# Optimization experiments

Hardware: AMD Instinct MI355X
Metric: run time of the kernel (lower is better)

The kernel has to match this reference:

```python
import jax, jax.numpy as jnp
import numpy as np

B, S, D = 2, 2048, 1024
H, HD = 16, 64  # num_attention_heads, attention_head_size


def setup_inputs() -> dict:
    key = jax.random.key(0)
    ks = jax.random.split(key, 8)
    std = 0.02
    return {
        "hidden_states": jax.random.normal(ks[0], (B, S, D), dtype=jnp.float32),
        "attention_mask": jnp.zeros((B, 1, 1, S), dtype=jnp.float32),
        "Wq": jax.random.normal(ks[1], (D, D), dtype=jnp.float32) * std,
        "bq": jnp.zeros((D,), dtype=jnp.float32),
        "Wk": jax.random.normal(ks[2], (D, D), dtype=jnp.float32) * std,
        "bk": jnp.zeros((D,), dtype=jnp.float32),
        "Wv": jax.random.normal(ks[3], (D, D), dtype=jnp.float32) * std,
        "bv": jnp.zeros((D,), dtype=jnp.float32),
    }


def reference(hidden_states, attention_mask, Wq, bq, Wk, bk, Wv, bv):
    b, s, d = hidden_states.shape

    def split_heads(x):  # [b,s,D] -> [b,H,s,HD]
        return x.reshape(b, s, H, HD).transpose(0, 2, 1, 3)

    q = split_heads(hidden_states @ Wq + bq)
    k = split_heads(hidden_states @ Wk + bk)
    v = split_heads(hidden_states @ Wv + bv)

    scores = jnp.einsum("bhqd,bhkd->bhqk", q, k) / jnp.sqrt(jnp.float32(HD))
    scores = scores + attention_mask  # additive mask, broadcast [b,1,1,s]
    probs = jax.nn.softmax(scores, axis=-1)  # dropout is identity at inference
    ctx = jnp.einsum("bhqk,bhkd->bhqd", probs, v)
    out = ctx.transpose(0, 2, 1, 3).reshape(b, s, d)
    return out
```

## Files before the change

### kernel.cpp

```cpp
#include <hip/hip_runtime.h>
#include <math.h>

#define CB 2
#define CS 2048
#define CD 1024
#define CH 16
#define CHD 64
#define CM (CB*CS)

#define QSCALE 0.18033688f
#define LOG2E  1.44269504f
#define BLOG   40.0f

typedef unsigned short u16;
using bf16x8 = __attribute__((ext_vector_type(8))) short;
using u16x8  = __attribute__((ext_vector_type(8))) unsigned short;
using f32x4  = __attribute__((ext_vector_type(4))) float;

__device__ __forceinline__ u16 f2bf(float f) {
    unsigned int u = __float_as_uint(f);
    u = (u + 0x7FFFu + ((u >> 16) & 1u)) >> 16;
    return (u16)u;
}

__device__ __forceinline__ unsigned cvt_pk_bf16(float lo, float hi) {
    unsigned r;
    asm("v_cvt_pk_bf16_f32 %0, %1, %2" : "=v"(r) : "v"(lo), "v"(hi));
    return r;
}

__device__ __forceinline__ void load_lds16(const u16* g, u16* l) {
    __builtin_amdgcn_global_load_lds(
        (const __attribute__((address_space(1))) unsigned int*)g,
        (__attribute__((address_space(3))) unsigned int*)l, 16, 0, 0);
}

__global__ __launch_bounds__(256)
void convert_all(const float* __restrict__ X, u16* __restrict__ Xb,
                 const float* __restrict__ Wq, const float* __restrict__ Wk,
                 const float* __restrict__ Wv, u16* __restrict__ Wt)
{
    const int bid = blockIdx.x;
    const int tid = threadIdx.x;

    if (bid < 2048) {
        size_t i = ((size_t)bid * 256 + tid) * 8;
        float4 v0 = *(const float4*)(X + i);
        float4 v1 = *(const float4*)(X + i + 4);
        u16x8 o;
        o[0] = f2bf(v0.x); o[1] = f2bf(v0.y); o[2] = f2bf(v0.z); o[3] = f2bf(v0.w);
        o[4] = f2bf(v1.x); o[5] = f2bf(v1.y); o[6] = f2bf(v1.z); o[7] = f2bf(v1.w);
        *(u16x8*)(Xb + i) = o;
        return;
    }

    const int r3 = bid - 2048;
    const int z  = r3 >> 8;
    const int bx = r3 & 15;
    const int by = (r3 >> 4) & 15;
    const float* W = (z == 0) ? Wq : (z == 1) ? Wk : Wv;
    const float sc = (z == 0) ? QSCALE : 1.0f;
    u16* Wo = Wt + (size_t)z * CD * CD;

    __shared__ u16 T[64][72];
    const int k0 = bx << 6;
    const int n0 = by << 6;

    #pragma unroll
    for (int it = 0; it < 4; ++it) {
        int r = (tid >> 4) + (it << 4);
        int c = (tid & 15) << 2;
        float4 v = *(const float4*)(W + (size_t)(k0 + r) * CD + n0 + c);
        T[c + 0][r] = f2bf(v.x * sc);
        T[c + 1][r] = f2bf(v.y * sc);
        T[c + 2][r] = f2bf(v.z * sc);
        T[c + 3][r] = f2bf(v.w * sc);
    }
    __syncthreads();
    #pragma unroll
    for (int it = 0; it < 2; ++it) {
        int cc = tid + (it << 8);
        int n  = cc >> 3;
        int ch = (cc & 7) << 3;
        *(uint4*)(Wo + (size_t)(n0 + n) * CD + k0 + ch) = *(const uint4*)&T[n][ch];
    }
}

__global__ __launch_bounds__(256, 4)
void qkv_gemm_mfma(const u16* __restrict__ Xb, const u16* __restrict__ Wt,
                   const float* __restrict__ bq, const float* __restrict__ bk,
                   const float* __restrict__ bv,
                   u16* __restrict__ Qb, u16* __restrict__ Kb,
                   u16* __restrict__ Vt)
{
    const int flat = blockIdx.x + (blockIdx.y << 5) + (blockIdx.z << 8);
    const int nf   = (flat & 7) * 96 + (flat >> 3);
    const int bx   = nf & 31;
    const int by   = (nf >> 5) & 7;
    const int z    = nf >> 8;

    const u16* W = Wt + (size_t)z * CD * CD;
    const float* bias = (z == 0) ? bq : (z == 1) ? bk : bv;
    const float bscale = (z == 0) ? QSCALE : 1.0f;

    __shared__ u16 smem[17408];
    u16* As = smem;
    u16* Bs = smem + 8192;

    const int tid  = threadIdx.x;
    const int w    = tid >> 6;
    const int l    = tid & 63;
    const int l15  = l & 15;
    const int quad = l >> 4;
    const int wm   = w >> 1;
    const int wn   = w & 1;

    const int row0 = bx << 7;
    const int n0   = by << 7;

    f32x4 acc[4][4];
    #pragma unroll
    for (int mi = 0; mi < 4; ++mi)
        #pragma unroll
        for (int nt = 0; nt < 4; ++nt)
            acc[mi][nt] = (f32x4){0.f, 0.f, 0.f, 0.f};

    const u16* Ag = Xb + (size_t)row0 * CD;
    const u16* Bg = W  + (size_t)n0   * CD;
    const int lr8 = l >> 3;
    const int ls  = l & 7;
    const int lg  = (ls ^ lr8) << 3;
    const int q7  = l15 & 7;

    for (int k0 = 0; k0 < CD; k0 += 64) {
        __syncthreads();
        #pragma unroll
        for (int i = 0; i < 4; ++i) {
            int r = w * 32 + 8 * i + lr8;
            load_lds16(Ag + (size_t)r * CD + k0 + lg, As + (size_t)(w * 32 + 8 * i) * 64);
            load_lds16(Bg + (size_t)r * CD + k0 + lg, Bs + (size_t)(w * 32 + 8 * i) * 64);
        }
        __syncthreads();

        #pragma unroll
        for (int kk = 0; kk < 2; ++kk) {
            bf16x8 af[4], bfr[4];
            #pragma unroll
            for (int mi = 0; mi < 4; ++mi)
                af[mi] = *(const bf16x8*)
                    &As[(wm * 64 + mi * 16 + l15) * 64 + (((kk * 4 + quad) ^ q7) << 3)];
            #pragma unroll
            for (int nt = 0; nt < 4; ++nt)
                bfr[nt] = *(const bf16x8*)
                    &Bs[(wn * 64 + nt * 16 + l15) * 64 + (((kk * 4 + quad) ^ q7) << 3)];
            #pragma unroll
            for (int mi = 0; mi < 4; ++mi)
                #pragma unroll
                for (int nt = 0; nt < 4; ++nt)
                    acc[mi][nt] = __builtin_amdgcn_mfma_f32_16x16x32_bf16(
                        af[mi], bfr[nt], acc[mi][nt], 0, 0, 0);
        }
    }

    __syncthreads();

    u16 (*Ct)[136] = (u16(*)[136])smem;

    if (z < 2) {
        u16* Og = (z == 0) ? Qb : Kb;
        float bb[4];
        #pragma unroll
        for (int nt = 0; nt < 4; ++nt)
            bb[nt] = bias[n0 + wn * 64 + nt * 16 + l15] * bscale;

        #pragma unroll
        for (int nt = 0; nt < 4; ++nt)
            #pragma unroll
            for (int mi = 0; mi < 4; ++mi)
                #pragma unroll
                for (int r = 0; r < 4; ++r)
                    Ct[wm * 64 + mi * 16 + quad * 4 + r][wn * 64 + nt * 16 + l15] =
                        f2bf(acc[mi][nt][r] + bb[nt]);
        __syncthreads();
        #pragma unroll
        for (int it = 0; it < 8; ++it) {
            int c  = tid + (it << 8);
            int rl = c >> 4;
            int ck = c & 15;
            uint4 d = *(const uint4*)&Ct[rl][ck * 8];
            int gcol = n0 + ck * 8;
            int h = gcol >> 6, hd = gcol & 63;
            int m = row0 + rl;
            int b = m >> 11, s = m & (CS - 1);
            *(uint4*)(Og + ((size_t)(b * CH + h) * CS + s) * CHD + hd) = d;
        }
    } else {
        #pragma unroll
        for (int nt = 0; nt < 4; ++nt) {
            int col = n0 + wn * 64 + nt * 16 + l15;
            float bb = bias[col];
            #pragma unroll
            for (int mi = 0; mi < 4; ++mi)
                #pragma unroll
                for (int r = 0; r < 4; ++r) {
                    int ml = wm * 64 + mi * 16 + quad * 4 + r;
                    Ct[wn * 64 + nt * 16 + l15][ml] = f2bf(acc[mi][nt][r] + bb);
                }
        }
        __syncthreads();
        #pragma unroll
        for (int it = 0; it < 8; ++it) {
            int c   = tid + (it << 8);
            int dvl = c >> 4;
            int ch  = c & 15;
            uint4 vdat = *(const uint4*)&Ct[dvl][ch * 8];
            int col = n0 + dvl;
            int h   = col >> 6;
            int dv  = col & 63;
            int m0  = row0 + ch * 8;
            int b   = m0 >> 11;
            int s0  = m0 & (CS - 1);
            *(uint4*)(Vt + (((size_t)(b * CH + h)) * CHD + dv) * CS + s0) = vdat;
        }
    }
}

__global__ __launch_bounds__(512, 4)
void attn_mfma(const u16* __restrict__ Qg, const u16* __restrict__ Kg,
               const u16* __restrict__ Vtg, const float* __restrict__ mask,
               float* __restrict__ out)
{
    __shared__ u16 smem[32768];
    u16* KstB = smem;
    u16* VstB = smem + 8192;
    u16* PlB  = smem + 16384;

    const int flat = blockIdx.y * 16 + blockIdx.x;
    const int nf   = ((flat & 7) << 6) + (flat >> 3);
    const int q0   = (nf & 15) << 7;
    const int bh   = nf >> 4;
    const int b    = bh >> 4;
    const int h    = bh & 15;

    const int tid = threadIdx.x;
    const int w    = tid >> 6;
    const int qh   = w & 3;
    const int kh   = w >> 2;
    const int l    = tid & 63;
    const int l15  = l & 15;
    const int quad = l >> 4;
    const int q7   = l15 & 7;
    const int lr8  = l >> 3;
    const int lg   = ((l & 7) ^ lr8) << 3;

    const u16* Qp     = Qg  + (size_t)bh * CS * CHD;
    const u16* Kph    = Kg  + (size_t)bh * CS * CHD + ((size_t)(kh << 10)) * CHD;
    const u16* Vph    = Vtg + (size_t)bh * CHD * CS + (kh << 10);
    const float* mrh  = mask + (size_t)b * CS + (kh << 10);

    u16* Kst = KstB + kh * 4096;
    u16* Vst = VstB + kh * 4096;
    u16* Pw  = PlB  + w * 2048;

    bf16x8 qf[2][2];
    #pragma unroll
    for (int nq = 0; nq < 2; ++nq)
        #pragma unroll
        for (int hh = 0; hh < 2; ++hh)
            qf[nq][hh] = *(const bf16x8*)(
                Qp + (size_t)(q0 + qh * 32 + nq * 16 + l15) * CHD + hh * 32 + quad * 8);

    float lsum[2] = {0.f, 0.f};
    f32x4 O[2][4];
    #pragma unroll
    for (int nq = 0; nq < 2; ++nq)
        #pragma unroll
        for (int dt = 0; dt < 4; ++dt)
            O[nq][dt] = (f32x4){0.f, 0.f, 0.f, 0.f};

    for (int kt = 0; kt < 16; ++kt) {
        const int k0 = kt << 6;
        __syncthreads();
        #pragma unroll
        for (int i = 0; i < 2; ++i) {
            int rl = qh * 16 + 8 * i;
            load_lds16(Kph + (size_t)(k0 + rl + lr8) * CHD + lg, &Kst[rl * 64]);
            load_lds16(Vph + (size_t)(rl + lr8) * CS + k0 + lg,  &Vst[rl * 64]);
        }
        __syncthreads();

        bf16x8 kf[4][2];
        #pragma unroll
        for (int mt = 0; mt < 4; ++mt)
            #pragma unroll
            for (int hh = 0; hh < 2; ++hh)
                kf[mt][hh] = *(const bf16x8*)
                    &Kst[(mt * 16 + l15) * 64 + (((hh * 4 + quad) ^ q7) << 3)];

        f32x4 mc[4];
        #pragma unroll
        for (int mt = 0; mt < 4; ++mt) {
            f32x4 mv = *(const f32x4*)(mrh + k0 + mt * 16 + quad * 4);
            #pragma unroll
            for (int r = 0; r < 4; ++r)
                mc[mt][r] = fmaf(mv[r], LOG2E, -BLOG);
        }

        #pragma unroll
        for (int nq = 0; nq < 2; ++nq) {
            f32x4 st[4];
            #pragma unroll
            for (int mt = 0; mt < 4; ++mt) {
                f32x4 c0 = mc[mt];
                c0 = __builtin_amdgcn_mfma_f32_16x16x32_bf16(kf[mt][0], qf[nq][0], c0, 0, 0, 0);
                st[mt] = __builtin_amdgcn_mfma_f32_16x16x32_bf16(kf[mt][1], qf[nq][1], c0, 0, 0, 0);
            }
            float rs = lsum[nq];
            #pragma unroll
            for (int mt = 0; mt < 4; ++mt) {
                #pragma unroll
                for (int r = 0; r < 4; ++r) {
                    st[mt][r] = exp2f(st[mt][r]);
                    rs += st[mt][r];
                }
                int g = 2 * mt + (quad >> 1);
                int addr = (nq * 16 + l15) * 64 + ((g ^ q7) << 3) + ((quad & 1) << 2);
                uint2 d;
                d.x = cvt_pk_bf16(st[mt][0], st[mt][1]);
                d.y = cvt_pk_bf16(st[mt][2], st[mt][3]);
                *(uint2*)&Pw[addr] = d;
            }
            lsum[nq] = rs;
        }

        bf16x8 pf[2][2];
        #pragma unroll
        for (int nq = 0; nq < 2; ++nq)
            #pragma unroll
            for (int hh = 0; hh < 2; ++hh)
                pf[nq][hh] = *(const bf16x8*)
                    &Pw[(nq * 16 + l15) * 64 + (((hh * 4 + quad) ^ q7) << 3)];

        bf16x8 vf[4][2];
        #pragma unroll
        for (int dt = 0; dt < 4; ++dt)
            #pragma unroll
            for (int hh = 0; hh < 2; ++hh)
                vf[dt][hh] = *(const bf16x8*)
                    &Vst[(dt * 16 + l15) * 64 + (((hh * 4 + quad) ^ q7) << 3)];

        #pragma unroll
        for (int nq = 0; nq < 2; ++nq)
            #pragma unroll
            for (int dt = 0; dt < 4; ++dt) {
                O[nq][dt] = __builtin_amdgcn_mfma_f32_16x16x32_bf16(
                    pf[nq][0], vf[dt][0], O[nq][dt], 0, 0, 0);
                O[nq][dt] = __builtin_amdgcn_mfma_f32_16x16x32_bf16(
                    pf[nq][1], vf[dt][1], O[nq][dt], 0, 0, 0);
            }
    }

    #pragma unroll
    for (int nq = 0; nq < 2; ++nq) {
        lsum[nq] += __shfl_xor(lsum[nq], 16);
        lsum[nq] += __shfl_xor(lsum[nq], 32);
    }

    __syncthreads();
    float* ob   = (float*)smem;
    float* lbuf = (float*)PlB;

    if (kh == 1) {
        float* obw = ob + qh * 2048;
        #pragma unroll
        for (int nq = 0; nq < 2; ++nq)
            #pragma unroll
            for (int dt = 0; dt < 4; ++dt)
                #pragma unroll
                for (int r = 0; r < 4; ++r)
                    obw[(nq * 16 + quad * 4 + r) * 64 + dt * 16 + l15] = O[nq][dt][r];
        if (quad == 0) {
            lbuf[qh * 32 + l15]      = lsum[0];
            lbuf[qh * 32 + 16 + l15] = lsum[1];
        }
    }
    __syncthreads();

    if (kh == 0) {
        const float* obw = ob + qh * 2048;
        #pragma unroll
        for (int nq = 0; nq < 2; ++nq) {
            float inv = 1.0f / (lsum[nq] + lbuf[qh * 32 + nq * 16 + l15]);
            #pragma unroll
            for (int r = 0; r < 4; ++r) {
                float invr = __shfl(inv, quad * 4 + r);
                int q = q0 + qh * 32 + nq * 16 + quad * 4 + r;
                float* orow = out + ((size_t)b * CS + q) * CD + h * CHD;
                #pragma unroll
                for (int dt = 0; dt < 4; ++dt)
                    orow[dt * 16 + l15] =
                        (O[nq][dt][r] + obw[(nq * 16 + quad * 4 + r) * 64 + dt * 16 + l15]) * invr;
            }
        }
    }
}

extern "C" void kernel_launch(void* const* d_in, const int* in_sizes, int n_in,
                              void* d_out, int out_size, void* d_ws, size_t ws_size,
                              hipStream_t stream)
{
    const float* X    = (const float*)d_in[0];
    const float* mask = (const float*)d_in[1];
    const float* Wq   = (const float*)d_in[2];
    const float* bq   = (const float*)d_in[3];
    const float* Wk   = (const float*)d_in[4];
    const float* bk   = (const float*)d_in[5];
    const float* Wv   = (const float*)d_in[6];
    const float* bv   = (const float*)d_in[7];
    float* out = (float*)d_out;

    char* ws = (char*)d_ws;
    u16* Xb = (u16*)(ws);
    u16* Wt = (u16*)(ws + ((size_t)8  << 20));
    u16* Qb = (u16*)(ws + ((size_t)14 << 20));
    u16* Kb = (u16*)(ws + ((size_t)22 << 20));
    u16* Vt = (u16*)(ws + ((size_t)30 << 20));

    convert_all<<<2048 + 768, 256, 0, stream>>>(X, Xb, Wq, Wk, Wv, Wt);
    qkv_gemm_mfma<<<dim3(CM / 128, CD / 128, 3), 256, 0, stream>>>(
        Xb, Wt, bq, bk, bv, Qb, Kb, Vt);
    attn_mfma<<<dim3(CS / 128, CB * CH), 512, 0, stream>>>(Qb, Kb, Vt, mask, out);
}
```

Before: 181.0 us.

## Rewrite QKV GEMM as 256x256 double-buffered tile with 8 waves and interleaved loads

The QKV projection GEMM moves from 128x128 tiles on 4 waves to 256x256 tiles on 8 waves. It adds double-buffered LDS (128 KB) so the next K-slice is fetched while MFMAs run on the current one, using manual barriers and s_setprio around the MFMA groups. This is meant to raise arithmetic intensity per block and hide global load latency. In exchange the grid shrinks to 192 blocks, which may underfill the CUs, and register and LDS pressure go up. The epilogue is split into two halves to fit the shared-memory staging.

```diff
diff --git a/kernel.cpp b/kernel.cpp
--- a/kernel.cpp
+++ b/kernel.cpp
@@ -86,141 +86,202 @@
     }
 }
 
-__global__ __launch_bounds__(256, 4)
+
+#define GBAR() asm volatile("s_barrier" ::: "memory")
+#define GVMC0() asm volatile("s_waitcnt vmcnt(0)" ::: "memory")
+
+#define GSTAGE(KS, AD, BD, PART)                                              \
+    {                                                                         \
+        const int rb = ((PART) << 7) + (w << 4);                              \
+        _Pragma("unroll")                                                     \
+        for (int j = 0; j < 2; ++j) {                                         \
+            load_lds16(Ag + (size_t)(rb + (j << 3) + lr8) * CD + ((KS) << 6) + lg, \
+                       (AD) + (rb + (j << 3)) * 64);                          \
+            load_lds16(Bg + (size_t)(rb + (j << 3) + lr8) * CD + ((KS) << 6) + lg, \
+                       (BD) + (rb + (j << 3)) * 64);                          \
+        }                                                                     \
+    }
+
+#define RD_AF(AC, MHH)                                                        \
+    _Pragma("unroll")                                                         \
+    for (int mi = 0; mi < 4; ++mi)                                            \
+        _Pragma("unroll")                                                     \
+        for (int kk = 0; kk < 2; ++kk)                                        \
+            af[mi][kk] = *(const bf16x8*)&(AC)[                               \
+                (wm * 128 + (MHH) * 64 + mi * 16 + l15) * 64 +                \
+                (((kk * 4 + quad) ^ q7) << 3)];
+
+#define RD_BF(BC, NHH, DST)                                                   \
+    _Pragma("unroll")                                                         \
+    for (int nt = 0; nt < 2; ++nt)                                            \
+        _Pragma("unroll")                                                     \
+        for (int kk = 0; kk < 2; ++kk)                                        \
+            DST[nt][kk] = *(const bf16x8*)&(BC)[                              \
+                (wn * 64 + (NHH) * 32 + nt * 16 + l15) * 64 +                 \
+                (((kk * 4 + quad) ^ q7) << 3)];
+
+#define GMM(MHH, NHH, BFH)                                                    \
+    _Pragma("unroll")                                                         \
+    for (int mi = 0; mi < 4; ++mi)                                            \
+        _Pragma("unroll")                                                     \
+        for (int nt = 0; nt < 2; ++nt) {                                      \
+            acc[(MHH)*4+mi][(NHH)*2+nt] = __builtin_amdgcn_mfma_f32_16x16x32_bf16( \
+                af[mi][0], BFH[nt][0], acc[(MHH)*4+mi][(NHH)*2+nt], 0, 0, 0); \
+            acc[(MHH)*4+mi][(NHH)*2+nt] = __builtin_amdgcn_mfma_f32_16x16x32_bf16( \
+                af[mi][1], BFH[nt][1], acc[(MHH)*4+mi][(NHH)*2+nt], 0, 0, 0); \
+        }
+
+#define KSTEP(KT, AC, BC, AD, BD, LAST)                                       \
+    {                                                                         \
+                                                     \
+        RD_AF(AC, 0); RD_BF(BC, 0, bf0);                                      \
+        if (!(LAST)) GSTAGE((KT) + 1, AD, BD, 0);                             \
+        GBAR(); __builtin_amdgcn_s_setprio(1); GMM(0, 0, bf0);                \
+        __builtin_amdgcn_s_setprio(0); GBAR();                                \
+                                                     \
+        RD_BF(BC, 1, bf1);                                                    \
+        if (!(LAST)) GSTAGE((KT) + 1, AD, BD, 1);                             \
+        GBAR(); __builtin_amdgcn_s_setprio(1); GMM(0, 1, bf1);                \
+        __builtin_amdgcn_s_setprio(0); GBAR();                                \
+                                                     \
+        RD_AF(AC, 1);                                                         \
+        GBAR(); __builtin_amdgcn_s_setprio(1); GMM(1, 1, bf1);                \
+        __builtin_amdgcn_s_setprio(0); GBAR();                                \
+             \
+        __builtin_amdgcn_s_setprio(1); GMM(1, 0, bf0);                        \
+        __builtin_amdgcn_s_setprio(0); GVMC0(); GBAR();                       \
+    }
+
+__global__ __launch_bounds__(512, 2)
 void qkv_gemm_mfma(const u16* __restrict__ Xb, const u16* __restrict__ Wt,
                    const float* __restrict__ bq, const float* __restrict__ bk,
                    const float* __restrict__ bv,
                    u16* __restrict__ Qb, u16* __restrict__ Kb,
                    u16* __restrict__ Vt)
 {
-    const int flat = blockIdx.x + (blockIdx.y << 5) + (blockIdx.z << 8);
-    const int nf   = (flat & 7) * 96 + (flat >> 3);
-    const int bx   = nf & 31;
-    const int by   = (nf >> 5) & 7;
-    const int z    = nf >> 8;
-
-    const u16* W = Wt + (size_t)z * CD * CD;
+    __shared__ u16 smem[65536];
+    u16* As0 = smem;
+    u16* Bs0 = smem + 16384;
+    u16* As1 = smem + 32768;
+    u16* Bs1 = smem + 49152;
+
+    const int flat = blockIdx.x + blockIdx.y * 16;
+    const int nf   = (flat & 7) * 24 + (flat >> 3);
+    const int bx   = nf & 15;
+    const int by   = nf >> 4;
+    const int z    = by >> 2;
+
     const float* bias = (z == 0) ? bq : (z == 1) ? bk : bv;
     const float bscale = (z == 0) ? QSCALE : 1.0f;
-
-    __shared__ u16 smem[17408];
-    u16* As = smem;
-    u16* Bs = smem + 8192;
 
     const int tid  = threadIdx.x;
     const int w    = tid >> 6;
     const int l    = tid & 63;
     const int l15  = l & 15;
     const int quad = l >> 4;
-    const int wm   = w >> 1;
-    const int wn   = w & 1;
-
-    const int row0 = bx << 7;
-    const int n0   = by << 7;
-
-    f32x4 acc[4][4];
-    #pragma unroll
-    for (int mi = 0; mi < 4; ++mi)
+    const int q7   = l15 & 7;
+    const int lr8  = l >> 3;
+    const int lg   = ((l & 7) ^ lr8) << 3;
+    const int wm   = w >> 2;
+    const int wn   = w & 3;
+
+    const u16* Ag = Xb + (size_t)(bx << 8) * CD;
+    const u16* Bg = Wt + (size_t)(by << 8) * CD;
+
+    f32x4 acc[8][4];
+    #pragma unroll
+    for (int mi = 0; mi < 8; ++mi)
         #pragma unroll
         for (int nt = 0; nt < 4; ++nt)
             acc[mi][nt] = (f32x4){0.f, 0.f, 0.f, 0.f};
 
-    const u16* Ag = Xb + (size_t)row0 * CD;
-    const u16* Bg = W  + (size_t)n0   * CD;
-    const int lr8 = l >> 3;
-    const int ls  = l & 7;
-    const int lg  = (ls ^ lr8) << 3;
-    const int q7  = l15 & 7;
-
-    for (int k0 = 0; k0 < CD; k0 += 64) {
-        __syncthreads();
-        #pragma unroll
-        for (int i = 0; i < 4; ++i) {
-            int r = w * 32 + 8 * i + lr8;
-            load_lds16(Ag + (size_t)r * CD + k0 + lg, As + (size_t)(w * 32 + 8 * i) * 64);
-            load_lds16(Bg + (size_t)r * CD + k0 + lg, Bs + (size_t)(w * 32 + 8 * i) * 64);
-        }
-        __syncthreads();
-
-        #pragma unroll
-        for (int kk = 0; kk < 2; ++kk) {
-            bf16x8 af[4], bfr[4];
-            #pragma unroll
-            for (int mi = 0; mi < 4; ++mi)
-                af[mi] = *(const bf16x8*)
-                    &As[(wm * 64 + mi * 16 + l15) * 64 + (((kk * 4 + quad) ^ q7) << 3)];
-            #pragma unroll
-            for (int nt = 0; nt < 4; ++nt)
-                bfr[nt] = *(const bf16x8*)
-                    &Bs[(wn * 64 + nt * 16 + l15) * 64 + (((kk * 4 + quad) ^ q7) << 3)];
-            #pragma unroll
-            for (int mi = 0; mi < 4; ++mi)
-                #pragma unroll
-                for (int nt = 0; nt < 4; ++nt)
-                    acc[mi][nt] = __builtin_amdgcn_mfma_f32_16x16x32_bf16(
-                        af[mi], bfr[nt], acc[mi][nt], 0, 0, 0);
-        }
-    }
-
-    __syncthreads();
-
-    u16 (*Ct)[136] = (u16(*)[136])smem;
+    bf16x8 af[4][2], bf0[2][2], bf1[2][2];
+
+    GSTAGE(0, As0, Bs0, 0);
+    GSTAGE(0, As0, Bs0, 1);
+    GVMC0(); GBAR();
+
+    #pragma unroll 1
+    for (int kt = 0; kt < 16; kt += 2) {
+        KSTEP(kt,     As0, Bs0, As1, Bs1, false);
+        KSTEP(kt + 1, As1, Bs1, As0, Bs0, (kt + 1) == 15);
+    }
+
+    const int bycol = (by & 3) << 8;
 
     if (z < 2) {
         u16* Og = (z == 0) ? Qb : Kb;
         float bb[4];
         #pragma unroll
         for (int nt = 0; nt < 4; ++nt)
-            bb[nt] = bias[n0 + wn * 64 + nt * 16 + l15] * bscale;
-
-        #pragma unroll
-        for (int nt = 0; nt < 4; ++nt)
-            #pragma unroll
-            for (int mi = 0; mi < 4; ++mi)
+            bb[nt] = bias[bycol + wn * 64 + nt * 16 + l15] * bscale;
+
+        u16 (*Ct)[264] = (u16(*)[264])smem;
+        #pragma unroll
+        for (int mh = 0; mh < 2; ++mh) {
+            __syncthreads();
+            if (wm == mh) {
                 #pragma unroll
-                for (int r = 0; r < 4; ++r)
-                    Ct[wm * 64 + mi * 16 + quad * 4 + r][wn * 64 + nt * 16 + l15] =
-                        f2bf(acc[mi][nt][r] + bb[nt]);
-        __syncthreads();
-        #pragma unroll
-        for (int it = 0; it < 8; ++it) {
-            int c  = tid + (it << 8);
-            int rl = c >> 4;
-            int ck = c & 15;
-            uint4 d = *(const uint4*)&Ct[rl][ck * 8];
-            int gcol = n0 + ck * 8;
-            int h = gcol >> 6, hd = gcol & 63;
-            int m = row0 + rl;
-            int b = m >> 11, s = m & (CS - 1);
-            *(uint4*)(Og + ((size_t)(b * CH + h) * CS + s) * CHD + hd) = d;
+                for (int MH2 = 0; MH2 < 2; ++MH2)
+                    #pragma unroll
+                    for (int nt = 0; nt < 4; ++nt)
+                        #pragma unroll
+                        for (int mi = 0; mi < 4; ++mi)
+                            #pragma unroll
+                            for (int r = 0; r < 4; ++r)
+                                Ct[MH2 * 64 + mi * 16 + quad * 4 + r]
+                                  [wn * 64 + nt * 16 + l15] =
+                                    f2bf(acc[MH2 * 4 + mi][nt][r] + bb[nt]);
+            }
+            __syncthreads();
+            #pragma unroll
+            for (int it = 0; it < 8; ++it) {
+                int c  = tid + (it << 9);
+                int rl = c >> 5;
+                int ck = c & 31;
+                uint4 d = *(const uint4*)&Ct[rl][ck * 8];
+                int gcol = bycol + ck * 8;
+                int h = gcol >> 6, hd = gcol & 63;
+                int m = (bx << 8) + (mh << 7) + rl;
+                int b = m >> 11, s = m & (CS - 1);
+                *(uint4*)(Og + ((size_t)(b * CH + h) * CS + s) * CHD + hd) = d;
+            }
         }
     } else {
-        #pragma unroll
-        for (int nt = 0; nt < 4; ++nt) {
-            int col = n0 + wn * 64 + nt * 16 + l15;
-            float bb = bias[col];
-            #pragma unroll
-            for (int mi = 0; mi < 4; ++mi)
+        u16 (*Ctv)[136] = (u16(*)[136])smem;
+        #pragma unroll
+        for (int mh = 0; mh < 2; ++mh) {
+            __syncthreads();
+            if (wm == mh) {
                 #pragma unroll
-                for (int r = 0; r < 4; ++r) {
-                    int ml = wm * 64 + mi * 16 + quad * 4 + r;
-                    Ct[wn * 64 + nt * 16 + l15][ml] = f2bf(acc[mi][nt][r] + bb);
+                for (int nt = 0; nt < 4; ++nt) {
+                    int col = wn * 64 + nt * 16 + l15;
+                    float bbv = bias[bycol + col];
+                    #pragma unroll
+                    for (int MH2 = 0; MH2 < 2; ++MH2)
+                        #pragma unroll
+                        for (int mi = 0; mi < 4; ++mi)
+                            #pragma unroll
+                            for (int r = 0; r < 4; ++r)
+                                Ctv[col][MH2 * 64 + mi * 16 + quad * 4 + r] =
+                                    f2bf(acc[MH2 * 4 + mi][nt][r] + bbv);
                 }
-        }
-        __syncthreads();
-        #pragma unroll
-        for (int it = 0; it < 8; ++it) {
-            int c   = tid + (it << 8);
-            int dvl = c >> 4;
-            int ch  = c & 15;
-            uint4 vdat = *(const uint4*)&Ct[dvl][ch * 8];
-            int col = n0 + dvl;
-            int h   = col >> 6;
-            int dv  = col & 63;
-            int m0  = row0 + ch * 8;
-            int b   = m0 >> 11;
-            int s0  = m0 & (CS - 1);
-            *(uint4*)(Vt + (((size_t)(b * CH + h)) * CHD + dv) * CS + s0) = vdat;
+            }
+            __syncthreads();
+            #pragma unroll
+            for (int it = 0; it < 8; ++it) {
+                int c   = tid + (it << 9);
+                int dvl = c >> 4;
+                int ch  = c & 15;
+                uint4 vdat = *(const uint4*)&Ctv[dvl][ch * 8];
+                int colg = bycol + dvl;
+                int h    = colg >> 6;
+                int dv   = colg & 63;
+                int m0   = (bx << 8) + (mh << 7) + ch * 8;
+                int b    = m0 >> 11;
+                int s0   = m0 & (CS - 1);
+                *(uint4*)(Vt + (((size_t)(b * CH + h)) * CHD + dv) * CS + s0) = vdat;
+            }
         }
     }
 }
@@ -427,7 +488,7 @@
     u16* Vt = (u16*)(ws + ((size_t)30 << 20));
 
     convert_all<<<2048 + 768, 256, 0, stream>>>(X, Xb, Wq, Wk, Wv, Wt);
-    qkv_gemm_mfma<<<dim3(CM / 128, CD / 128, 3), 256, 0, stream>>>(
+    qkv_gemm_mfma<<<dim3(16, 12), 512, 0, stream>>>(
         Xb, Wt, bq, bk, bv, Qb, Kb, Vt);
     attn_mfma<<<dim3(CS / 128, CB * CH), 512, 0, stream>>>(Qb, Kb, Vt, mask, out);
 }
```

Measured after the change: 183.7 us. About the same (+1.5%).
